# Kernel tuning notes

Hardware: AMD Instinct MI355X
Metric: run time of the kernel (lower is better)

Reference implementation:

```python
import jax, jax.numpy as jnp
import numpy as np

N, H, F = 131072, 256, 4096
MIN_FRAG = 3
LN_EPS = 1e-5
NORM_EPS = 1e-12
CONSISTENCY_FACTOR = 0.03
INTERMOLECULAR_WEIGHT = 0.2
SCALING_FACTOR = 0.05  # initial_strength at epoch 0 (progressive schedule, eval mode)


def _normalize(x):
    # torch F.normalize(p=2, dim=1): x / max(||x||, eps)
    n = jnp.linalg.norm(x, axis=-1, keepdims=True)
    return x / jnp.maximum(n, NORM_EPS)


def _frag_consistency(feat, frag_ids, valid):
    # size-weighted sum of per-fragment mean deviations == mean deviation over valid atoms
    m = valid.astype(feat.dtype)[:, None]
    seg_sum = jax.ops.segment_sum(feat * m, frag_ids, num_segments=F)
    seg_cnt = jax.ops.segment_sum(m, frag_ids, num_segments=F)
    means = seg_sum / jnp.maximum(seg_cnt, 1.0)  # scatter-mean over valid atoms
    sim = jnp.sum(_normalize(feat) * _normalize(means)[frag_ids], axis=-1)  # [N]
    dev = (1.0 - sim) * valid.astype(feat.dtype)
    return jnp.sum(dev) / jnp.maximum(jnp.sum(valid.astype(feat.dtype)), 1.0)


def setup_inputs() -> dict:
    key = jax.random.key(0)
    ks = jax.random.split(key, 8)
    return {
        "scalar_short": jax.random.normal(ks[0], (N, H), jnp.float32),
        "scalar_long": jax.random.normal(ks[1], (N, H), jnp.float32),
        "vector_short": jax.random.normal(ks[2], (N, 3, H), jnp.float32),
        "vector_long": jax.random.normal(ks[3], (N, 3, H), jnp.float32),
        "fragment_ids": jax.random.randint(ks[4], (N,), 0, F, dtype=jnp.int32),
        "ln_gamma": jnp.ones((H,), jnp.float32),
        "ln_beta": jnp.zeros((H,), jnp.float32),
        "W1": jax.random.normal(ks[5], (H, H), jnp.float32) / np.sqrt(H),
        "b1": jnp.zeros((H,), jnp.float32),
        "Wv": jax.random.normal(ks[6], (H, H), jnp.float32) / np.sqrt(H),
    }


def reference(scalar_short, scalar_long, vector_short, vector_long, fragment_ids,
              ln_gamma, ln_beta, W1, b1, Wv):
    # valid_mask: atoms belonging to fragments of size >= MIN_FRAG
    sizes = jax.ops.segment_sum(jnp.ones((N,), jnp.float32), fragment_ids, num_segments=F)
    valid = sizes[fragment_ids] >= MIN_FRAG  # [N] bool

    # scalar_projector: LayerNorm -> Linear -> SiLU (dropout identity at eval)
    mu = jnp.mean(scalar_short, axis=-1, keepdims=True)
    var = jnp.var(scalar_short, axis=-1, keepdims=True)
    xh = (scalar_short - mu) / jnp.sqrt(var + LN_EPS) * ln_gamma + ln_beta
    scalar_features = jax.nn.silu(xh @ W1.T + b1)  # [N, H]

    intra = _frag_consistency(scalar_features, fragment_ids, valid)

    # vector branch: per-atom magnitude = mean over 3 spatial comps of ||.||_2 over hidden
    vec_mag = jnp.mean(jnp.linalg.norm(vector_short, axis=2), axis=1, keepdims=True)  # [N,1]
    # Linear(bias=False) on mag.expand(-1,H) then [:, :1] == silu(mag * sum(Wv[0,:]))
    w0 = jnp.sum(Wv[0])
    vector_features = jax.nn.silu(vec_mag * w0)  # [N,1]
    vec_loss = _frag_consistency(vector_features, fragment_ids, valid)

    # interfragment differentiation over ALL atoms (no valid mask)
    cnt = jax.ops.segment_sum(jnp.ones((N, 1), jnp.float32), fragment_ids, num_segments=F)
    sfrag = jax.ops.segment_sum(scalar_features, fragment_ids, num_segments=F) / jnp.maximum(cnt, 1.0)
    vfrag = jax.ops.segment_sum(vec_mag, fragment_ids, num_segments=F) / jnp.maximum(cnt, 1.0)
    combined = _normalize(jnp.concatenate([sfrag, vfrag], axis=1))  # [F, H+1]
    sim = combined @ combined.T  # [F, F]
    off_sum = jnp.sum(sim) - jnp.trace(sim)
    inter = off_sum / (F * F - F + 1e-6)

    total = intra + vec_loss + INTERMOLECULAR_WEIGHT * inter
    return CONSISTENCY_FACTOR * total * SCALING_FACTOR
```

## Files before the change

kernel.cpp:

```cpp
#include <hip/hip_runtime.h>
#include <hip/hip_bf16.h>
#include <stdint.h>

#define NA 131072
#define HD 256
#define NF 4096
#define MINFRAG 3
#define LN_EPS 1e-5f
#define NEPS 1e-12f

#define OFF_CNT    0ull
#define OFF_VSUM   16384ull
#define OFF_VFSUM  32768ull
#define OFF_NVSUM  49152ull
#define OFF_FILL   65536ull
#define OFF_DBL    81920ull
#define ZERO_BYTES 84008ull
#define OFF_OFFS   86016ull
#define OFF_SVEC   102400ull
#define OFF_C0     103424ull
#define OFF_W0     104448ull
#define OFF_RNORM  131072ull
#define OFF_ORDER  655360ull
#define OFF_GBF    1179648ull
#define OFF_SSUM   1310720ull
#define OFF_NSUM   5505024ull
#define OFF_FEAT   9699328ull

#define IDX_TRACE 257
#define IDX_DEVS  258
#define IDX_DEVV  259
#define IDX_VCNT  260

typedef __attribute__((ext_vector_type(8))) short short8;
typedef __attribute__((ext_vector_type(4))) float f32x4;
union F4S8 { float4 f; short8 s; };
union BFU { __hip_bfloat16 b; unsigned short u; };

__device__ __forceinline__ unsigned short f2b(float x) {
    BFU t; t.b = __float2bfloat16(x); return t.u;
}
__device__ __forceinline__ float b2f(unsigned short u) {
    return __uint_as_float(((uint32_t)u) << 16);
}
__device__ __forceinline__ float wredsum(float v) {
#pragma unroll
    for (int m = 32; m; m >>= 1) v += __shfl_xor(v, m, 64);
    return v;
}
__device__ __forceinline__ float silu_f(float x) { return x / (1.f + expf(-x)); }

__global__ __launch_bounds__(256) void k_prep(
    const float* __restrict__ W1, const float* __restrict__ gamma,
    const float* __restrict__ beta, const float* __restrict__ b1,
    const float* __restrict__ Wv,
    unsigned short* __restrict__ Gbf, float* __restrict__ svec,
    float* __restrict__ c0, float* __restrict__ w0) {
    __shared__ float red[8];
    int o = blockIdx.x;
    int t = threadIdx.x;
    if (o < HD) {
        float w = W1[(size_t)o * HD + t];
        unsigned short gb = f2b(w * gamma[t]);
        Gbf[(size_t)o * HD + t] = gb;
        float sp = b2f(gb);
        float cp = w * beta[t];
#pragma unroll
        for (int m = 32; m; m >>= 1) { sp += __shfl_xor(sp, m, 64); cp += __shfl_xor(cp, m, 64); }
        int wv = t >> 6;
        if ((t & 63) == 0) { red[wv] = sp; red[4 + wv] = cp; }
        __syncthreads();
        if (t == 0) {
            svec[o] = red[0] + red[1] + red[2] + red[3];
            c0[o]   = red[4] + red[5] + red[6] + red[7] + b1[o];
        }
    } else {
        float v = Wv[t];
#pragma unroll
        for (int m = 32; m; m >>= 1) v += __shfl_xor(v, m, 64);
        int wv = t >> 6;
        if ((t & 63) == 0) red[wv] = v;
        __syncthreads();
        if (t == 0) w0[0] = red[0] + red[1] + red[2] + red[3];
    }
}

__global__ __launch_bounds__(256) void k_stats(
    const float* __restrict__ vs, const int* __restrict__ fid,
    const float* __restrict__ w0p,
    int* __restrict__ cnt, float* __restrict__ vsum,
    float* __restrict__ vfsum, float* __restrict__ nvsum) {
    int gwave = (blockIdx.x * blockDim.x + threadIdx.x) >> 6;
    int lane = threadIdx.x & 63;
    int nw = (gridDim.x * blockDim.x) >> 6;
    float w0 = w0p[0];
    for (int i = gwave; i < NA; i += nw) {
        const float* base = vs + (size_t)i * 3 * HD;
        float4 v0 = ((const float4*)(base))[lane];
        float4 v1 = ((const float4*)(base + HD))[lane];
        float4 v2 = ((const float4*)(base + 2 * HD))[lane];
        float q0 = v0.x * v0.x + v0.y * v0.y + v0.z * v0.z + v0.w * v0.w;
        float q1 = v1.x * v1.x + v1.y * v1.y + v1.z * v1.z + v1.w * v1.w;
        float q2 = v2.x * v2.x + v2.y * v2.y + v2.z * v2.z + v2.w * v2.w;
#pragma unroll
        for (int m = 32; m; m >>= 1) {
            q0 += __shfl_xor(q0, m, 64);
            q1 += __shfl_xor(q1, m, 64);
            q2 += __shfl_xor(q2, m, 64);
        }
        if (lane == 0) {
            float vm = (sqrtf(q0) + sqrtf(q1) + sqrtf(q2)) * (1.f / 3.f);
            float vf = silu_f(vm * w0);
            float nv = vf / fmaxf(fabsf(vf), NEPS);
            int f = fid[i];
            atomicAdd(&cnt[f], 1);
            atomicAdd(&vsum[f], vm);
            atomicAdd(&vfsum[f], vf);
            atomicAdd(&nvsum[f], nv);
        }
    }
}

__global__ __launch_bounds__(256) void k_scan(const int* __restrict__ cnt,
                                              int* __restrict__ offs) {
    __shared__ int wsum[4];
    int t = threadIdx.x;
    int base = t * 16;
    int c[16];
    int tot = 0;
#pragma unroll
    for (int j = 0; j < 16; ++j) { c[j] = cnt[base + j]; tot += c[j]; }
    int lane = t & 63, w = t >> 6;
    int v = tot;
#pragma unroll
    for (int d = 1; d < 64; d <<= 1) {
        int o = __shfl_up(v, d, 64);
        if (lane >= d) v += o;
    }
    if (lane == 63) wsum[w] = v;
    __syncthreads();
    int wbase = 0;
    for (int i = 0; i < w; ++i) wbase += wsum[i];
    int run = wbase + v - tot;
#pragma unroll
    for (int j = 0; j < 16; ++j) { offs[base + j] = run; run += c[j]; }
}

__global__ __launch_bounds__(256) void k_scatter(
    const int* __restrict__ fid, const int* __restrict__ offs,
    int* __restrict__ fill, int* __restrict__ order) {
    int i = blockIdx.x * blockDim.x + threadIdx.x;
    if (i < NA) {
        int f = fid[i];
        int p = atomicAdd(&fill[f], 1);
        order[offs[f] + p] = i;
    }
}

__global__ __launch_bounds__(256) void k_gemm(
    const float* __restrict__ A, const unsigned short* __restrict__ Gbf,
    const float* __restrict__ svec, const float* __restrict__ c0,
    unsigned short* __restrict__ feat, float* __restrict__ rnorm) {
    __shared__ float4 As16[64 * 8];
    __shared__ float4 Bs16[256 * 8];
    __shared__ float muS[64], rsS[64];
    __shared__ float sqL[64][4];

    int tid = threadIdx.x;
    int lane = tid & 63, wid = tid >> 6;
    int r0 = blockIdx.x * 64;
    int rowT = tid >> 4;
    int c4 = tid & 15;

    f32x4 acc[4][4] = {};
    float s1p[4] = {0, 0, 0, 0}, s2p[4] = {0, 0, 0, 0};

    for (int k0 = 0; k0 < HD; k0 += 64) {
#pragma unroll
        for (int p = 0; p < 4; ++p) {
            int row = 16 * p + rowT;
            float4 v = *(const float4*)(A + (size_t)(r0 + row) * HD + k0 + c4 * 4);
            s1p[p] += v.x + v.y + v.z + v.w;
            s2p[p] += v.x * v.x + v.y * v.y + v.z * v.z + v.w * v.w;
            ushort4 pk;
            pk.x = f2b(v.x); pk.y = f2b(v.y); pk.z = f2b(v.z); pk.w = f2b(v.w);
            int slot = row * 8 + ((c4 >> 1) ^ (row & 7));
            ((ushort4*)&As16[slot])[c4 & 1] = pk;
        }
#pragma unroll
        for (int p = 0; p < 8; ++p) {
            int u = p * 256 + tid;
            int n = u >> 3, cc = u & 7;
            float4 g = *(const float4*)(Gbf + (size_t)n * HD + k0 + cc * 8);
            Bs16[n * 8 + (cc ^ (n & 7))] = g;
        }
        __syncthreads();
#pragma unroll
        for (int kk = 0; kk < 2; ++kk) {
            int uo = kk * 4 + (lane >> 4);
            short8 a[4], b[4];
#pragma unroll
            for (int mi = 0; mi < 4; ++mi) {
                int r = mi * 16 + (lane & 15);
                F4S8 t_; t_.f = As16[r * 8 + (uo ^ (r & 7))];
                a[mi] = t_.s;
            }
#pragma unroll
            for (int ni = 0; ni < 4; ++ni) {
                int n = wid * 64 + ni * 16 + (lane & 15);
                F4S8 t_; t_.f = Bs16[n * 8 + (uo ^ (n & 7))];
                b[ni] = t_.s;
            }
#pragma unroll
            for (int mi = 0; mi < 4; ++mi)
#pragma unroll
                for (int ni = 0; ni < 4; ++ni)
                    acc[mi][ni] = __builtin_amdgcn_mfma_f32_16x16x32_bf16(
                        a[mi], b[ni], acc[mi][ni], 0, 0, 0);
        }
        __syncthreads();
    }
#pragma unroll
    for (int p = 0; p < 4; ++p) {
        float s1 = s1p[p], s2 = s2p[p];
#pragma unroll
        for (int m = 1; m < 16; m <<= 1) {
            s1 += __shfl_xor(s1, m, 64);
            s2 += __shfl_xor(s2, m, 64);
        }
        if (c4 == 0) {
            int row = 16 * p + rowT;
            float mu_ = s1 * (1.f / HD);
            float var = s2 * (1.f / HD) - mu_ * mu_;
            muS[row] = mu_;
            rsS[row] = rsqrtf(var + LN_EPS);
        }
    }
    __syncthreads();
    float sv[4], cv[4];
#pragma unroll
    for (int ni = 0; ni < 4; ++ni) {
        int c = wid * 64 + ni * 16 + (lane & 15);
        sv[ni] = svec[c];
        cv[ni] = c0[c];
    }
    float sq[4][4];
#pragma unroll
    for (int mi = 0; mi < 4; ++mi)
#pragma unroll
        for (int q = 0; q < 4; ++q) {
            int rl = mi * 16 + (lane >> 4) * 4 + q;
            float mu_ = muS[rl], rs_ = rsS[rl];
            size_t ro = (size_t)(r0 + rl) * HD;
            float sqa = 0.f;
#pragma unroll
            for (int ni = 0; ni < 4; ++ni) {
                float pre = rs_ * (acc[mi][ni][q] - mu_ * sv[ni]) + cv[ni];
                unsigned short us = f2b(silu_f(pre));
                feat[ro + wid * 64 + ni * 16 + (lane & 15)] = us;
                float fr = b2f(us);
                sqa += fr * fr;
            }
            sq[mi][q] = sqa;
        }
#pragma unroll
    for (int mi = 0; mi < 4; ++mi)
#pragma unroll
        for (int q = 0; q < 4; ++q) {
            float s_ = sq[mi][q];
            s_ += __shfl_xor(s_, 1, 64);
            s_ += __shfl_xor(s_, 2, 64);
            s_ += __shfl_xor(s_, 4, 64);
            s_ += __shfl_xor(s_, 8, 64);
            if ((lane & 15) == 0) sqL[mi * 16 + (lane >> 4) * 4 + q][wid] = s_;
        }
    __syncthreads();
    if (tid < 64) {
        float t = sqL[tid][0] + sqL[tid][1] + sqL[tid][2] + sqL[tid][3];
        rnorm[r0 + tid] = 1.f / fmaxf(sqrtf(t), NEPS);
    }
}

__global__ __launch_bounds__(256) void k_ssum(
    const unsigned short* __restrict__ feat, const float* __restrict__ rnorm,
    const int* __restrict__ order, const int* __restrict__ offs,
    const int* __restrict__ cnt, float* __restrict__ ssum,
    float* __restrict__ nsum) {
    int wid = threadIdx.x >> 6, lane = threadIdx.x & 63;
    int f = blockIdx.x * 4 + wid;
    int base = offs[f], n = cnt[f];
    float4 as = {0.f, 0.f, 0.f, 0.f};
    float4 an = {0.f, 0.f, 0.f, 0.f};
    for (int a0 = 0; a0 < n; a0 += 64) {
        int idx = 0;
        float rn = 0.f;
        if (a0 + lane < n) {
            idx = order[base + a0 + lane];
            rn = rnorm[idx];
        }
        int m = n - a0; if (m > 64) m = 64;
        for (int j = 0; j < m; ++j) {
            int i = __shfl(idx, j, 64);
            float r = __shfl(rn, j, 64);
            ushort4 u = *(const ushort4*)(feat + (size_t)i * HD + lane * 4);
            float f0 = b2f(u.x), f1 = b2f(u.y), f2 = b2f(u.z), f3 = b2f(u.w);
            as.x += f0; as.y += f1; as.z += f2; as.w += f3;
            an.x = fmaf(f0, r, an.x); an.y = fmaf(f1, r, an.y);
            an.z = fmaf(f2, r, an.z); an.w = fmaf(f3, r, an.w);
        }
    }
    *(float4*)(ssum + (size_t)f * HD + lane * 4) = as;
    *(float4*)(nsum + (size_t)f * HD + lane * 4) = an;
}

__global__ __launch_bounds__(256) void k_frag(
    const float* __restrict__ ssum, const float* __restrict__ nsum,
    const int* __restrict__ cnt, const float* __restrict__ vsum,
    const float* __restrict__ vfsum, const float* __restrict__ nvsum,
    double* __restrict__ dbl) {
    int gwave = (blockIdx.x * blockDim.x + threadIdx.x) >> 6;
    int lane = threadIdx.x & 63;
    int nw = (gridDim.x * blockDim.x) >> 6;

    double la0 = 0, la1 = 0, la2 = 0, la3 = 0;
    double lv = 0, ltr = 0, lvc = 0, ldS = 0, ldV = 0;

    for (int f = gwave; f < NF; f += nw) {
        float4 s = ((const float4*)(ssum + (size_t)f * HD))[lane];
        float4 nn = ((const float4*)(nsum + (size_t)f * HD))[lane];
        int c = cnt[f];
        float ssq = s.x * s.x + s.y * s.y + s.z * s.z + s.w * s.w;
        float dsn = nn.x * s.x + nn.y * s.y + nn.z * s.z + nn.w * s.w;
#pragma unroll
        for (int m = 32; m; m >>= 1) {
            ssq += __shfl_xor(ssq, m, 64);
            dsn += __shfl_xor(dsn, m, 64);
        }
        float inv_all = 1.f / fmaxf((float)c, 1.f);
        float m0 = s.x * inv_all, m1 = s.y * inv_all, m2 = s.z * inv_all, m3 = s.w * inv_all;
        float ssq_mean = ssq * inv_all * inv_all;
        float vfr = vsum[f] * inv_all;
        float nrm2 = ssq_mean + vfr * vfr;
        float inv = 1.f / fmaxf(sqrtf(nrm2), NEPS);
        la0 += (double)(m0 * inv);
        la1 += (double)(m1 * inv);
        la2 += (double)(m2 * inv);
        la3 += (double)(m3 * inv);
        if (lane == 0) {
            lv += (double)(vfr * inv);
            ltr += (double)(nrm2 * inv * inv);
            if (c >= MINFRAG) {
                lvc += (double)c;
                float denom = fmaxf(sqrtf(ssq), NEPS);
                ldS += (double)c - (double)(dsn / denom);
                float vfm = vfsum[f] * inv_all;
                float vsgn = vfm / fmaxf(fabsf(vfm), NEPS);
                ldV += (double)c - (double)(vsgn * nvsum[f]);
            }
        }
    }
    atomicAdd(&dbl[4 * lane + 0], la0);
    atomicAdd(&dbl[4 * lane + 1], la1);
    atomicAdd(&dbl[4 * lane + 2], la2);
    atomicAdd(&dbl[4 * lane + 3], la3);
    if (lane == 0) {
        atomicAdd(&dbl[256], lv);
        atomicAdd(&dbl[IDX_TRACE], ltr);
        atomicAdd(&dbl[IDX_VCNT], lvc);
        atomicAdd(&dbl[IDX_DEVS], ldS);
        atomicAdd(&dbl[IDX_DEVV], ldV);
    }
}

__global__ __launch_bounds__(64) void k_final(const double* __restrict__ dbl,
                                              float* __restrict__ out) {
    if (threadIdx.x == 0 && blockIdx.x == 0) {
        double s2 = 0;
        for (int d = 0; d < 257; ++d) s2 += dbl[d] * dbl[d];
        double off = s2 - dbl[IDX_TRACE];
        double inter = off / ((double)NF * NF - NF + 1e-6);
        double vc = fmax(dbl[IDX_VCNT], 1.0);
        double total = dbl[IDX_DEVS] / vc + dbl[IDX_DEVV] / vc + 0.2 * inter;
        out[0] = (float)(0.03 * 0.05 * total);
    }
}

extern "C" void kernel_launch(void* const* d_in, const int* in_sizes, int n_in,
                              void* d_out, int out_size, void* d_ws, size_t ws_size,
                              hipStream_t stream) {
    const float* scalar_short = (const float*)d_in[0];
    const float* vector_short = (const float*)d_in[2];
    const int* fragment_ids = (const int*)d_in[4];
    const float* ln_gamma = (const float*)d_in[5];
    const float* ln_beta = (const float*)d_in[6];
    const float* W1 = (const float*)d_in[7];
    const float* b1 = (const float*)d_in[8];
    const float* Wv = (const float*)d_in[9];
    float* out = (float*)d_out;

    char* ws = (char*)d_ws;
    int* cnt = (int*)(ws + OFF_CNT);
    float* vsum = (float*)(ws + OFF_VSUM);
    float* vfsum = (float*)(ws + OFF_VFSUM);
    float* nvsum = (float*)(ws + OFF_NVSUM);
    int* fill = (int*)(ws + OFF_FILL);
    double* dbl = (double*)(ws + OFF_DBL);
    int* offs = (int*)(ws + OFF_OFFS);
    float* svec = (float*)(ws + OFF_SVEC);
    float* c0 = (float*)(ws + OFF_C0);
    float* w0 = (float*)(ws + OFF_W0);
    float* rnorm = (float*)(ws + OFF_RNORM);
    int* order = (int*)(ws + OFF_ORDER);
    unsigned short* Gbf = (unsigned short*)(ws + OFF_GBF);
    float* ssum = (float*)(ws + OFF_SSUM);
    float* nsum = (float*)(ws + OFF_NSUM);
    unsigned short* feat = (unsigned short*)(ws + OFF_FEAT);

    hipMemsetAsync(ws, 0, ZERO_BYTES, stream);
    k_prep<<<HD + 1, 256, 0, stream>>>(W1, ln_gamma, ln_beta, b1, Wv, Gbf, svec, c0, w0);
    k_stats<<<2048, 256, 0, stream>>>(vector_short, fragment_ids, w0, cnt, vsum, vfsum, nvsum);
    k_scan<<<1, 256, 0, stream>>>(cnt, offs);
    k_scatter<<<NA / 256, 256, 0, stream>>>(fragment_ids, offs, fill, order);
    k_gemm<<<NA / 64, 256, 0, stream>>>(scalar_short, Gbf, svec, c0, feat, rnorm);
    k_ssum<<<NF / 4, 256, 0, stream>>>(feat, rnorm, order, offs, cnt, ssum, nsum);
    k_frag<<<64, 256, 0, stream>>>(ssum, nsum, cnt, vsum, vfsum, nvsum, dbl);
    k_final<<<1, 64, 0, stream>>>(dbl, out);
}
```

Measured before the change: 256.6 us.

## Fuse fragment segment-sum into GEMM epilogue using fragment-sorted row order

The GEMM now reads scalar rows in fragment-sorted order (through the order array) and reduces each block's 64 output rows per fragment in shared memory. It writes ssum/nsum directly when a fragment lies entirely inside the block and uses atomics for fragments that span block edges. This removes the bf16 feature buffer round trip, the rnorm buffer and the separate k_ssum kernel. In exchange the A-matrix loads become row gathers, the memset grows to zero ssum/nsum, and float atomics make the result order-dependent at fragment boundaries.

```diff
diff --git a/kernel.cpp b/kernel.cpp
--- a/kernel.cpp
+++ b/kernel.cpp
@@ -15,17 +15,15 @@
 #define OFF_NVSUM  49152ull
 #define OFF_FILL   65536ull
 #define OFF_DBL    81920ull
-#define ZERO_BYTES 84008ull
-#define OFF_OFFS   86016ull
-#define OFF_SVEC   102400ull
-#define OFF_C0     103424ull
-#define OFF_W0     104448ull
-#define OFF_RNORM  131072ull
-#define OFF_ORDER  655360ull
-#define OFF_GBF    1179648ull
-#define OFF_SSUM   1310720ull
-#define OFF_NSUM   5505024ull
-#define OFF_FEAT   9699328ull
+#define OFF_SSUM   86016ull
+#define OFF_NSUM   4280320ull
+#define ZERO_BYTES 8474624ull
+#define OFF_OFFS   8474624ull
+#define OFF_SVEC   8491008ull
+#define OFF_C0     8492032ull
+#define OFF_W0     8493056ull
+#define OFF_GBF    8493568ull
+#define OFF_ORDER  8624640ull
 
 #define IDX_TRACE 257
 #define IDX_DEVS  258
@@ -42,11 +40,6 @@
 }
 __device__ __forceinline__ float b2f(unsigned short u) {
     return __uint_as_float(((uint32_t)u) << 16);
-}
-__device__ __forceinline__ float wredsum(float v) {
-#pragma unroll
-    for (int m = 32; m; m >>= 1) v += __shfl_xor(v, m, 64);
-    return v;
 }
 __device__ __forceinline__ float silu_f(float x) { return x / (1.f + expf(-x)); }
 
@@ -160,11 +153,14 @@
 __global__ __launch_bounds__(256) void k_gemm(
     const float* __restrict__ A, const unsigned short* __restrict__ Gbf,
     const float* __restrict__ svec, const float* __restrict__ c0,
-    unsigned short* __restrict__ feat, float* __restrict__ rnorm) {
+    const int* __restrict__ order, const int* __restrict__ fid,
+    const int* __restrict__ offs, const int* __restrict__ cnt,
+    float* __restrict__ ssum, float* __restrict__ nsum) {
     __shared__ float4 As16[64 * 8];
     __shared__ float4 Bs16[256 * 8];
-    __shared__ float muS[64], rsS[64];
+    __shared__ float muS[64], rsS[64], rnS[64];
     __shared__ float sqL[64][4];
+    __shared__ int fragS[64];
 
     int tid = threadIdx.x;
     int lane = tid & 63, wid = tid >> 6;
@@ -172,6 +168,17 @@
     int rowT = tid >> 4;
     int c4 = tid & 15;
 
+    if (tid < 64) {
+        int gi = order[r0 + tid];
+        muS[tid] = __int_as_float(gi);
+        fragS[tid] = fid[gi];
+    }
+    __syncthreads();
+    int rid[4];
+#pragma unroll
+    for (int p = 0; p < 4; ++p) rid[p] = __float_as_int(muS[16 * p + rowT]);
+    __syncthreads();
+
     f32x4 acc[4][4] = {};
     float s1p[4] = {0, 0, 0, 0}, s2p[4] = {0, 0, 0, 0};
 
@@ -179,7 +186,7 @@
 #pragma unroll
         for (int p = 0; p < 4; ++p) {
             int row = 16 * p + rowT;
-            float4 v = *(const float4*)(A + (size_t)(r0 + row) * HD + k0 + c4 * 4);
+            float4 v = *(const float4*)(A + (size_t)rid[p] * HD + k0 + c4 * 4);
             s1p[p] += v.x + v.y + v.z + v.w;
             s2p[p] += v.x * v.x + v.y * v.y + v.z * v.z + v.w * v.w;
             ushort4 pk;
@@ -244,6 +251,7 @@
         sv[ni] = svec[c];
         cv[ni] = c0[c];
     }
+    unsigned short* featS = (unsigned short*)Bs16;
     float sq[4][4];
 #pragma unroll
     for (int mi = 0; mi < 4; ++mi)
@@ -251,13 +259,13 @@
         for (int q = 0; q < 4; ++q) {
             int rl = mi * 16 + (lane >> 4) * 4 + q;
             float mu_ = muS[rl], rs_ = rsS[rl];
-            size_t ro = (size_t)(r0 + rl) * HD;
             float sqa = 0.f;
 #pragma unroll
             for (int ni = 0; ni < 4; ++ni) {
+                int c = wid * 64 + ni * 16 + (lane & 15);
                 float pre = rs_ * (acc[mi][ni][q] - mu_ * sv[ni]) + cv[ni];
                 unsigned short us = f2b(silu_f(pre));
-                feat[ro + wid * 64 + ni * 16 + (lane & 15)] = us;
+                featS[rl * 256 + (c ^ ((rl & 7) << 2))] = us;
                 float fr = b2f(us);
                 sqa += fr * fr;
             }
@@ -277,40 +285,39 @@
     __syncthreads();
     if (tid < 64) {
         float t = sqL[tid][0] + sqL[tid][1] + sqL[tid][2] + sqL[tid][3];
-        rnorm[r0 + tid] = 1.f / fmaxf(sqrtf(t), NEPS);
-    }
-}
-
-__global__ __launch_bounds__(256) void k_ssum(
-    const unsigned short* __restrict__ feat, const float* __restrict__ rnorm,
-    const int* __restrict__ order, const int* __restrict__ offs,
-    const int* __restrict__ cnt, float* __restrict__ ssum,
-    float* __restrict__ nsum) {
-    int wid = threadIdx.x >> 6, lane = threadIdx.x & 63;
-    int f = blockIdx.x * 4 + wid;
-    int base = offs[f], n = cnt[f];
-    float4 as = {0.f, 0.f, 0.f, 0.f};
-    float4 an = {0.f, 0.f, 0.f, 0.f};
-    for (int a0 = 0; a0 < n; a0 += 64) {
-        int idx = 0;
-        float rn = 0.f;
-        if (a0 + lane < n) {
-            idx = order[base + a0 + lane];
-            rn = rnorm[idx];
-        }
-        int m = n - a0; if (m > 64) m = 64;
-        for (int j = 0; j < m; ++j) {
-            int i = __shfl(idx, j, 64);
-            float r = __shfl(rn, j, 64);
-            ushort4 u = *(const ushort4*)(feat + (size_t)i * HD + lane * 4);
-            float f0 = b2f(u.x), f1 = b2f(u.y), f2 = b2f(u.z), f3 = b2f(u.w);
-            as.x += f0; as.y += f1; as.z += f2; as.w += f3;
-            an.x = fmaf(f0, r, an.x); an.y = fmaf(f1, r, an.y);
-            an.z = fmaf(f2, r, an.z); an.w = fmaf(f3, r, an.w);
-        }
-    }
-    *(float4*)(ssum + (size_t)f * HD + lane * 4) = as;
-    *(float4*)(nsum + (size_t)f * HD + lane * 4) = an;
+        rnS[tid] = 1.f / fmaxf(sqrtf(t), NEPS);
+    }
+    __syncthreads();
+    int cc = wid * 64 + lane;
+    float sAcc = 0.f, nAcc = 0.f;
+    int curF = fragS[0];
+    for (int row = 0; row < 64; ++row) {
+        int f = fragS[row];
+        if (f != curF) {
+            int gs = offs[curF], n = cnt[curF];
+            if (gs >= r0 && gs + n <= r0 + 64) {
+                ssum[(size_t)curF * HD + cc] = sAcc;
+                nsum[(size_t)curF * HD + cc] = nAcc;
+            } else {
+                atomicAdd(&ssum[(size_t)curF * HD + cc], sAcc);
+                atomicAdd(&nsum[(size_t)curF * HD + cc], nAcc);
+            }
+            sAcc = 0.f; nAcc = 0.f; curF = f;
+        }
+        float v = b2f(featS[row * 256 + (cc ^ ((row & 7) << 2))]);
+        sAcc += v;
+        nAcc = fmaf(v, rnS[row], nAcc);
+    }
+    {
+        int gs = offs[curF], n = cnt[curF];
+        if (gs >= r0 && gs + n <= r0 + 64) {
+            ssum[(size_t)curF * HD + cc] = sAcc;
+            nsum[(size_t)curF * HD + cc] = nAcc;
+        } else {
+            atomicAdd(&ssum[(size_t)curF * HD + cc], sAcc);
+            atomicAdd(&nsum[(size_t)curF * HD + cc], nAcc);
+        }
+    }
 }
 
 __global__ __launch_bounds__(256) void k_frag(
@@ -405,24 +412,22 @@
     float* nvsum = (float*)(ws + OFF_NVSUM);
     int* fill = (int*)(ws + OFF_FILL);
     double* dbl = (double*)(ws + OFF_DBL);
+    float* ssum = (float*)(ws + OFF_SSUM);
+    float* nsum = (float*)(ws + OFF_NSUM);
     int* offs = (int*)(ws + OFF_OFFS);
     float* svec = (float*)(ws + OFF_SVEC);
     float* c0 = (float*)(ws + OFF_C0);
     float* w0 = (float*)(ws + OFF_W0);
-    float* rnorm = (float*)(ws + OFF_RNORM);
+    unsigned short* Gbf = (unsigned short*)(ws + OFF_GBF);
     int* order = (int*)(ws + OFF_ORDER);
-    unsigned short* Gbf = (unsigned short*)(ws + OFF_GBF);
-    float* ssum = (float*)(ws + OFF_SSUM);
-    float* nsum = (float*)(ws + OFF_NSUM);
-    unsigned short* feat = (unsigned short*)(ws + OFF_FEAT);
 
     hipMemsetAsync(ws, 0, ZERO_BYTES, stream);
     k_prep<<<HD + 1, 256, 0, stream>>>(W1, ln_gamma, ln_beta, b1, Wv, Gbf, svec, c0, w0);
     k_stats<<<2048, 256, 0, stream>>>(vector_short, fragment_ids, w0, cnt, vsum, vfsum, nvsum);
     k_scan<<<1, 256, 0, stream>>>(cnt, offs);
     k_scatter<<<NA / 256, 256, 0, stream>>>(fragment_ids, offs, fill, order);
-    k_gemm<<<NA / 64, 256, 0, stream>>>(scalar_short, Gbf, svec, c0, feat, rnorm);
-    k_ssum<<<NF / 4, 256, 0, stream>>>(feat, rnorm, order, offs, cnt, ssum, nsum);
+    k_gemm<<<NA / 64, 256, 0, stream>>>(scalar_short, Gbf, svec, c0, order,
+                                        fragment_ids, offs, cnt, ssum, nsum);
     k_frag<<<64, 256, 0, stream>>>(ssum, nsum, cnt, vsum, vfsum, nvsum, dbl);
     k_final<<<1, 64, 0, stream>>>(dbl, out);
 }
```

Result: no change. 252.7 us (-1.5%).
